# Performance work log

Hardware: AMD Instinct MI355X
Metric: run time of the kernel (lower is better)

Reference implementation:

```python
import jax, jax.numpy as jnp
from jax import lax
import numpy as np


def _gru_step(gi, h, Whh, bhh):
    # torch GRU cell: gates ordered (r, z, n); gi = x @ Wih.T + bih precomputed
    gh = h @ Whh.T + bhh
    ir, iz, inn = jnp.split(gi, 3, axis=-1)
    hr, hz, hn = jnp.split(gh, 3, axis=-1)
    r = jax.nn.sigmoid(ir + hr)
    z = jax.nn.sigmoid(iz + hz)
    n = jnp.tanh(inn + r * hn)
    return (1.0 - z) * n + z * h


def setup_inputs() -> dict:
    key = jax.random.key(0)
    ks = jax.random.split(key, 12)
    B, T, F, Wd, H, L = 64, 80, 4096, 6000, 512, 32
    s = 0.05  # weight init scale
    return {
        "x": jax.random.uniform(ks[0], (B, T, F), jnp.float32),  # nonneg CNN features -> full video lengths
        "y": jax.random.randint(ks[1], (L, B), 0, Wd),           # time-major caption token ids
        "Wih_v": jax.random.normal(ks[2], (3 * H, F), jnp.float32) * s,
        "Whh_v": jax.random.normal(ks[3], (3 * H, H), jnp.float32) * s,
        "bih_v": jax.random.normal(ks[4], (3 * H,), jnp.float32) * s,
        "bhh_v": jax.random.normal(ks[5], (3 * H,), jnp.float32) * s,
        "Wih_c": jax.random.normal(ks[6], (3 * H, H + Wd), jnp.float32) * s,
        "Whh_c": jax.random.normal(ks[7], (3 * H, H), jnp.float32) * s,
        "bih_c": jax.random.normal(ks[8], (3 * H,), jnp.float32) * s,
        "bhh_c": jax.random.normal(ks[9], (3 * H,), jnp.float32) * s,
        "Wout": jax.random.normal(ks[10], (Wd, H), jnp.float32) * s,
        "bout": jax.random.normal(ks[11], (Wd,), jnp.float32) * s,
    }


def reference(x, y, Wih_v, Whh_v, bih_v, bhh_v, Wih_c, Whh_c, bih_c, bhh_c, Wout, bout):
    B, T, F = x.shape
    L = y.shape[0]
    H = Whh_v.shape[1]
    Wd = Wout.shape[0]
    dt = x.dtype

    # ---- encode stage: video GRU over full-length sequences (time-major) ----
    xs = jnp.transpose(x, (1, 0, 2))                       # [T,B,F]
    gi_v = jnp.einsum('tbf,gf->tbg', xs, Wih_v) + bih_v    # precompute input gates
    h0 = jnp.zeros((B, H), dt)

    def enc_v(h, gi):
        h2 = _gru_step(gi, h, Whh_v, bhh_v)
        return h2, h2

    _, enc_out = lax.scan(enc_v, h0, gi_v)                 # [T,B,H]

    # caption GRU over [enc_out ; zeros(word_dim)]; zero word part contributes nothing
    Wih_c_h = Wih_c[:, :H]                                 # [3H,H]
    Wih_c_w = Wih_c[:, H:]                                 # [3H,Wd]
    gi_c = jnp.einsum('tbh,gh->tbg', enc_out, Wih_c_h) + bih_c

    def enc_c(h, gi):
        h2 = _gru_step(gi, h, Whh_c, bhh_c)
        return h2, None

    # NOTE: original code assigns this final hidden to `hidden_video` (quirk preserved)
    hidden_video, _ = lax.scan(enc_c, h0, gi_c)            # [B,H]

    # ---- decode stage: steps i = 1 .. L-1, zero frame input, teacher forcing ----
    gi_zero = jnp.broadcast_to(bih_v, (B, 3 * H))          # x=0 -> input gates are just bias
    WcwT = Wih_c_w.T                                       # [Wd,3H]; one-hot matmul == row gather

    def dec(h_v, y_prev):
        h_v2 = _gru_step(gi_zero, h_v, Whh_v, bhh_v)
        gi = h_v2 @ Wih_c_h.T + WcwT[y_prev] + bih_c       # concat([out, one_hot(y_prev)]) @ Wih_c.T
        h_c = _gru_step(gi, h_v2, Whh_c, bhh_c)            # initial hidden = fresh video hidden (original quirk)
        logits = h_c @ Wout.T + bout
        return h_v2, logits

    _, logits = lax.scan(dec, hidden_video, y[:-1])        # [L-1,B,Wd]

    probs = jnp.zeros((B, L, Wd), dt)
    probs = probs.at[0, 0, 1].set(1.0)                     # probs[0,:,1]=1 survives only at t=0
    probs = probs.at[:, 1:].set(jnp.transpose(logits, (1, 0, 2)))

    # loss is overwritten each iteration in the original -> last step only (cross-entropy)
    logp = jax.nn.log_softmax(logits[-1], axis=-1)         # [B,Wd]
    loss = -jnp.take_along_axis(logp, y[-1][:, None], axis=1).mean()
    return probs, loss
```

## Files before the change

### kernel.cpp

```cpp
#include <hip/hip_runtime.h>

typedef short s16x8 __attribute__((ext_vector_type(8)));
typedef float f32x4 __attribute__((ext_vector_type(4)));
typedef unsigned short u16x4 __attribute__((ext_vector_type(4)));

#define MFMA_B16(a, b, c) __builtin_amdgcn_mfma_f32_16x16x32_bf16((a), (b), (c), 0, 0, 0)

__device__ __forceinline__ unsigned short f2b(float f) {
    unsigned u = __builtin_bit_cast(unsigned, f);
    u = (u + 0x7fffu + ((u >> 16) & 1u)) >> 16;
    return (unsigned short)u;
}
__device__ __forceinline__ float b2f(unsigned short h) {
    unsigned u = ((unsigned)h) << 16;
    return __builtin_bit_cast(float, u);
}
__device__ __forceinline__ float sigm(float x) { return 1.f / (1.f + __expf(-x)); }
__device__ __forceinline__ float tanh_f(float x) {
    float t = __expf(-2.f * fabsf(x));
    float r = (1.f - t) / (1.f + t);
    return copysignf(r, x);
}

__device__ __forceinline__ void stg_b16_sc(unsigned short* p, unsigned short v) {
    unsigned v32 = v;
    asm volatile("global_store_short %0, %1, off sc1" :: "v"(p), "v"(v32) : "memory");
}
__device__ __forceinline__ void stg_b32_sc(float* p, float v) {
    asm volatile("global_store_dword %0, %1, off sc1" :: "v"(p), "v"(v) : "memory");
}
__device__ __forceinline__ unsigned long long ldg_u64_sc(const void* p) {
    return __hip_atomic_load((unsigned long long*)p, __ATOMIC_RELAXED, __HIP_MEMORY_SCOPE_AGENT);
}
__device__ __forceinline__ float ldg_b16_sc(const unsigned short* p) {
    unsigned short v = __hip_atomic_load((unsigned short*)p, __ATOMIC_RELAXED, __HIP_MEMORY_SCOPE_AGENT);
    return b2f(v);
}
__device__ __forceinline__ float ldg_f32_sc(const float* p) {
    return __hip_atomic_load((float*)p, __ATOMIC_RELAXED, __HIP_MEMORY_SCOPE_AGENT);
}
__device__ __forceinline__ s16x8 ldA_sc(const unsigned short* p) {
    union { unsigned long long u[2]; s16x8 v; } r;
    r.u[0] = ldg_u64_sc(p);
    r.u[1] = ldg_u64_sc((const unsigned long long*)p + 1);
    return r.v;
}

__device__ __forceinline__ void block_publish(int* flag, int v) {
    asm volatile("s_waitcnt vmcnt(0)" ::: "memory");
    __syncthreads();
    if (threadIdx.x == 0)
        __hip_atomic_store(flag, v, __ATOMIC_RELAXED, __HIP_MEMORY_SCOPE_AGENT);
}
template <int SLP>
__device__ __forceinline__ void flags_wait2(const int* f1, int t1, const int* f2, int t2) {
    const int lane = threadIdx.x & 63;
    const int* ptr = (lane < 32) ? (f1 + lane * 16) : (f2 + (lane - 32) * 16);
    const int tgt = (lane < 32) ? t1 : t2;
    for (;;) {
        int v = __hip_atomic_load((int*)ptr, __ATOMIC_RELAXED, __HIP_MEMORY_SCOPE_AGENT);
        if (__all(v >= tgt)) break;
        __builtin_amdgcn_s_sleep(SLP);
    }
}
template <int SLP>
__device__ __forceinline__ void flags_wait(const int* f, int t) {
    flags_wait2<SLP>(f, t, f, t);
}
template <int SLP>
__device__ __forceinline__ void scalar_wait(int* c, int target) {
    while (__hip_atomic_load(c, __ATOMIC_RELAXED, __HIP_MEMORY_SCOPE_AGENT) < target)
        __builtin_amdgcn_s_sleep(SLP);
}
__device__ __forceinline__ void wave_add(int* c) {
    asm volatile("s_waitcnt vmcnt(0)" ::: "memory");
    if ((threadIdx.x & 63) == 0)
        __hip_atomic_fetch_add(c, 1, __ATOMIC_RELAXED, __HIP_MEMORY_SCOPE_AGENT);
}

#define WTILE 8192
#define WF(Wl, t, c, lane) (*(const s16x8*)((Wl) + (((t) * 16 + (c)) * 64 + (lane)) * 8))

__device__ __forceinline__ void stage_swz(const unsigned short* __restrict__ src,
                                          unsigned short* dst) {
    for (int idx = threadIdx.x; idx < 1024; idx += 256) {
        const int ln = idx & 63;
        *(uint4*)(dst + (size_t)idx * 8) =
            *(const uint4*)(src + (size_t)(ln & 15) * 512 + (ln >> 4) * 8 + ((idx >> 6)) * 32);
    }
}

__device__ __forceinline__ void mm3_s(const unsigned short* __restrict__ A, int m0,
                                      const unsigned short* Wl, int lane,
                                      f32x4& a0, f32x4& a1, f32x4& a2) {
    const unsigned short* ab = A + (size_t)(m0 + (lane & 15)) * 512 + (lane >> 4) * 8;
#pragma unroll
    for (int c = 0; c < 16; ++c) {
        s16x8 a = ldA_sc(ab + c * 32);
        a0 = MFMA_B16(a, WF(Wl, 0, c, lane), a0);
        a1 = MFMA_B16(a, WF(Wl, 1, c, lane), a1);
        a2 = MFMA_B16(a, WF(Wl, 2, c, lane), a2);
    }
}
__device__ __forceinline__ void mm6_s(const unsigned short* __restrict__ A0,
                                      const unsigned short* __restrict__ A1, int m0,
                                      const unsigned short* Wl, int lane,
                                      f32x4& aR, f32x4& aZ, f32x4& aIN, f32x4& aHN) {
    const unsigned short* a0 = A0 + (size_t)(m0 + (lane & 15)) * 512 + (lane >> 4) * 8;
    const unsigned short* a1 = A1 + (size_t)(m0 + (lane & 15)) * 512 + (lane >> 4) * 8;
#pragma unroll
    for (int c = 0; c < 16; ++c) {
        s16x8 x0 = ldA_sc(a0 + c * 32);
        s16x8 x1 = ldA_sc(a1 + c * 32);
        aR  = MFMA_B16(x0, WF(Wl, 0, c, lane), aR);
        aZ  = MFMA_B16(x0, WF(Wl, 1, c, lane), aZ);
        aIN = MFMA_B16(x0, WF(Wl, 2, c, lane), aIN);
        aR  = MFMA_B16(x1, WF(Wl, 3, c, lane), aR);
        aZ  = MFMA_B16(x1, WF(Wl, 4, c, lane), aZ);
        aHN = MFMA_B16(x1, WF(Wl, 5, c, lane), aHN);
    }
}

__global__ void prep_kernel(const float* __restrict__ x, const float* __restrict__ Wih_v,
                            const float* __restrict__ Whh_v, const float* __restrict__ Whh_c,
                            const float* __restrict__ Wih_c, const float* __restrict__ Wout,
                            unsigned short* __restrict__ xB, unsigned short* __restrict__ WihB,
                            unsigned short* __restrict__ WhhvB, unsigned short* __restrict__ WhhcB,
                            unsigned short* __restrict__ WchhB, unsigned short* __restrict__ WoutB,
                            unsigned short* __restrict__ zeroB, int* __restrict__ ctrs,
                            float* __restrict__ out) {
    const int n = gridDim.x * blockDim.x;
    const int id0 = blockIdx.x * blockDim.x + threadIdx.x;
    for (int i = id0; i < 5242880; i += n) {
        const int e = i * 4;
        const int f = e & 4095, bt = e >> 12;
        const int b = bt / 80, t = bt - b * 80;
        float4 v = *(const float4*)(x + (size_t)e);
        u16x4 s = {f2b(v.x), f2b(v.y), f2b(v.z), f2b(v.w)};
        *(u16x4*)(xB + (size_t)(t * 64 + b) * 4096 + f) = s;
    }
    for (int i = id0; i < 1572864; i += n) {
        float4 v = *(const float4*)(Wih_v + (size_t)i * 4);
        u16x4 s = {f2b(v.x), f2b(v.y), f2b(v.z), f2b(v.w)};
        *(u16x4*)(WihB + (size_t)i * 4) = s;
    }
    for (int i = id0; i < 786432; i += n) {
        WhhvB[i] = f2b(Whh_v[i]);
        WhhcB[i] = f2b(Whh_c[i]);
        WchhB[i] = f2b(Wih_c[(size_t)(i >> 9) * 6512 + (i & 511)]);
    }
    for (int i = id0; i < 3072000; i += n) WoutB[i] = f2b(Wout[i]);
    for (int i = id0; i < 384000; i += n)
        out[(size_t)(i / 6000) * 192000 + (i % 6000)] = (i == 1) ? 1.f : 0.f;
    for (int i = id0; i < 32768; i += n) zeroB[i] = 0;
    for (int i = id0; i < 4096; i += n) ctrs[i] = 0;
}

__global__ __launch_bounds__(256) void gemm1_kernel(const unsigned short* __restrict__ xB,
                                                    const unsigned short* __restrict__ WihB,
                                                    const float* __restrict__ bih,
                                                    float* __restrict__ gi) {
    __shared__ unsigned short As[128 * 40];
    __shared__ unsigned short Bs[128 * 40];
    const int bm = blockIdx.x % 40;
    const int bn = blockIdx.x / 40;
    const int m0 = bm * 128, n0 = bn * 128;
    const int tid = threadIdx.x;
    const int lane = tid & 63;
    const int wave = tid >> 6;
    const int wm = (wave >> 1) * 64, wn = (wave & 1) * 64;
    const int quad = lane >> 4, l15 = lane & 15;

    const f32x4 z4 = {0.f, 0.f, 0.f, 0.f};
    f32x4 acc[4][4];
#pragma unroll
    for (int i = 0; i < 4; ++i)
#pragma unroll
        for (int j = 0; j < 4; ++j) acc[i][j] = z4;

    const int sr = tid >> 1;
    const int sc0 = (tid & 1) * 16;

    for (int k0 = 0; k0 < 4096; k0 += 32) {
        __syncthreads();
#pragma unroll
        for (int p = 0; p < 2; ++p) {
            const int c8 = sc0 + p * 8;
            *(s16x8*)&As[sr * 40 + c8] =
                *(const s16x8*)(xB + (size_t)(m0 + sr) * 4096 + k0 + c8);
            *(s16x8*)&Bs[sr * 40 + c8] =
                *(const s16x8*)(WihB + (size_t)(n0 + sr) * 4096 + k0 + c8);
        }
        __syncthreads();
        s16x8 af[4], bfr[4];
#pragma unroll
        for (int i = 0; i < 4; ++i) af[i] = *(const s16x8*)&As[(wm + i * 16 + l15) * 40 + quad * 8];
#pragma unroll
        for (int j = 0; j < 4; ++j) bfr[j] = *(const s16x8*)&Bs[(wn + j * 16 + l15) * 40 + quad * 8];
#pragma unroll
        for (int i = 0; i < 4; ++i)
#pragma unroll
            for (int j = 0; j < 4; ++j) acc[i][j] = MFMA_B16(af[i], bfr[j], acc[i][j]);
    }
#pragma unroll
    for (int i = 0; i < 4; ++i)
#pragma unroll
        for (int j = 0; j < 4; ++j)
#pragma unroll
            for (int r = 0; r < 4; ++r) {
                const int m = m0 + wm + i * 16 + quad * 4 + r;
                const int nn = n0 + wn + j * 16 + l15;
                gi[(size_t)m * 1536 + nn] = acc[i][j][r] + bih[nn];
            }
}

struct SeqParams {
    const float* bih_v; const float* bhh_v;
    const float* bih_c; const float* bhh_c;
    const float* bout;  const int* y;
    const float* gi;    const float* Wc;  float* out;
    const unsigned short* WhhvB; const unsigned short* WhhcB; const unsigned short* WchhB;
    const unsigned short* WoutB; unsigned short* WcwTB;
    unsigned short* eo;
    unsigned short* hv2B;
    float*          hv2F;
    unsigned short* hcdB;
    unsigned short* ecb0; unsigned short* ecb1; unsigned short* zeroB;
    float* hcf; float* lossP; int* ctr;
};
#define F_EO (p.ctr)
#define F_EC (p.ctr + 512)
#define F_HV (p.ctr + 1024)
#define F_HC (p.ctr + 1536)
#define S_TR (p.ctr + 2048)
#define S_LOG (p.ctr + 2064)
#define S_LP (p.ctr + 2080)

__global__ __launch_bounds__(256, 1) void seq_kernel(SeqParams p) {
    __shared__ unsigned short Wlds[49152];
    const int blk = blockIdx.x;
    const int lane = threadIdx.x & 63;
    const int wave = threadIdx.x >> 6;
    const int quad = lane >> 4, l15 = lane & 15;
    const f32x4 z4 = {0.f, 0.f, 0.f, 0.f};

    if (blk < 32) {
        const int j0 = blk * 16;
        const int j = j0 + l15;
        const int m0 = wave * 16;
        const int b_ = m0 + quad * 4;
#pragma unroll
        for (int g = 0; g < 3; ++g)
            stage_swz(p.WhhvB + (size_t)(g * 512 + j0) * 512, Wlds + g * WTILE);
        __syncthreads();
        const float bhr = p.bhh_v[j], bhz = p.bhh_v[512 + j], bhn = p.bhh_v[1024 + j];
        float hp[4] = {0.f, 0.f, 0.f, 0.f};

        for (int t = 0; t < 80; ++t) {
            float gr[4], gz[4], gn[4];
            const float* gt = p.gi + (size_t)t * 98304;
#pragma unroll
            for (int r = 0; r < 4; ++r) {
                const float* gb = gt + (size_t)(b_ + r) * 1536;
                gr[r] = gb[j]; gz[r] = gb[512 + j]; gn[r] = gb[1024 + j];
            }
            f32x4 aR = z4, aZ = z4, aN = z4;
            if (t > 0) {
                flags_wait<1>(F_EO, t);
                mm3_s(p.eo + (size_t)(t - 1) * 32768, m0, Wlds, lane, aR, aZ, aN);
            }
            unsigned short* eoW = p.eo + (size_t)t * 32768;
#pragma unroll
            for (int r = 0; r < 4; ++r) {
                float rg = sigm(gr[r] + aR[r] + bhr);
                float zg = sigm(gz[r] + aZ[r] + bhz);
                float ng = tanh_f(gn[r] + rg * (aN[r] + bhn));
                float hn = (1.f - zg) * ng + zg * hp[r];
                hp[r] = hn;
                stg_b16_sc(eoW + (size_t)(b_ + r) * 512 + j, f2b(hn));
            }
            block_publish(F_EO + blk * 16, t + 1);
        }

        flags_wait<1>(F_EC, 80);
        const float bir = p.bih_v[j], biz = p.bih_v[512 + j], bin_ = p.bih_v[1024 + j];
        for (int s = 0; s <= 30; ++s) {
            if (s > 0) flags_wait<1>(F_HV, s);
            f32x4 aR = z4, aZ = z4, aN = z4;
            mm3_s(p.hv2B + (size_t)s * 32768, m0, Wlds, lane, aR, aZ, aN);
            unsigned short* hw = p.hv2B + (size_t)(s + 1) * 32768;
            float* hwF = p.hv2F + (size_t)(s + 1) * 32768;
#pragma unroll
            for (int r = 0; r < 4; ++r) {
                float hpv = (s == 0) ? ldg_f32_sc(p.hcf + (size_t)(b_ + r) * 512 + j) : hp[r];
                float rg = sigm(bir + aR[r] + bhr);
                float zg = sigm(biz + aZ[r] + bhz);
                float ng = tanh_f(bin_ + rg * (aN[r] + bhn));
                float hn = (1.f - zg) * ng + zg * hpv;
                hp[r] = hn;
                stg_b16_sc(hw + (size_t)(b_ + r) * 512 + j, f2b(hn));
                stg_b32_sc(hwF + (size_t)(b_ + r) * 512 + j, hn);
            }
            block_publish(F_HV + blk * 16, s + 1);
        }

        if (blk < 16) {
            const int b = (blk << 2) | wave;
            scalar_wait<2>(S_LOG, 125);
            const float* lg = p.out + (size_t)b * 192000 + 186000;
            float m = -1e30f, sum = 0.f;
            for (int i = lane; i < 3000; i += 64) {
                union { unsigned long long u; float f[2]; } pr;
                pr.u = ldg_u64_sc(lg + 2 * i);
#pragma unroll
                for (int e = 0; e < 2; ++e) {
                    float v = pr.f[e];
                    float nm = fmaxf(m, v);
                    sum = sum * __expf(m - nm) + __expf(v - nm);
                    m = nm;
                }
            }
#pragma unroll
            for (int off = 32; off > 0; off >>= 1) {
                float m2 = __shfl_down(m, off);
                float s2 = __shfl_down(sum, off);
                float nm = fmaxf(m, m2);
                sum = sum * __expf(m - nm) + s2 * __expf(m2 - nm);
                m = nm;
            }
            if (lane == 0) {
                int yv = p.y[31 * 64 + b];
                float lgy = ldg_f32_sc(lg + yv);
                stg_b32_sc(p.lossP + b, (m + __logf(sum)) - lgy);
            }
            wave_add(S_LP);
            if (blk == 0 && wave == 0) {
                scalar_wait<1>(S_LP, 64);
                float v = ldg_f32_sc(p.lossP + lane);
#pragma unroll
                for (int off = 32; off > 0; off >>= 1) v += __shfl_down(v, off);
                if (lane == 0) p.out[12288000] = v * (1.f / 64.f);
            }
        }
    } else if (blk < 64) {
        const int cid = blk - 32;
        const int j0 = cid * 16;
        const int j = j0 + l15;
        const int m0 = wave * 16;
        const int b_ = m0 + quad * 4;
#pragma unroll
        for (int g = 0; g < 3; ++g) {
            stage_swz(p.WchhB + (size_t)(g * 512 + j0) * 512, Wlds + g * WTILE);
            stage_swz(p.WhhcB + (size_t)(g * 512 + j0) * 512, Wlds + (3 + g) * WTILE);
        }
        __syncthreads();
        const float bcr = p.bih_c[j] + p.bhh_c[j];
        const float bcz = p.bih_c[512 + j] + p.bhh_c[512 + j];
        const float bin_ = p.bih_c[1024 + j];
        const float bhn = p.bhh_c[1024 + j];
        float hp[4] = {0.f, 0.f, 0.f, 0.f};

        for (int t = 0; t < 80; ++t) {
            flags_wait2<1>(F_EO, t + 1, F_EC, t);
            const unsigned short* A1 = (t == 0) ? p.zeroB : ((t & 1) ? p.ecb0 : p.ecb1);
            unsigned short* ew = (t & 1) ? p.ecb1 : p.ecb0;
            f32x4 aR = z4, aZ = z4, aIN = z4, aHN = z4;
            mm6_s(p.eo + (size_t)t * 32768, A1, m0, Wlds, lane, aR, aZ, aIN, aHN);
#pragma unroll
            for (int r = 0; r < 4; ++r) {
                float rg = sigm(aR[r] + bcr);
                float zg = sigm(aZ[r] + bcz);
                float ng = tanh_f(aIN[r] + bin_ + rg * (aHN[r] + bhn));
                float hn = (1.f - zg) * ng + zg * hp[r];
                hp[r] = hn;
                unsigned short hb = f2b(hn);
                stg_b16_sc(ew + (size_t)(b_ + r) * 512 + j, hb);
                if (t == 79) {
                    stg_b16_sc(p.hv2B + (size_t)(b_ + r) * 512 + j, hb);
                    stg_b32_sc(p.hcf + (size_t)(b_ + r) * 512 + j, hn);
                }
            }
            block_publish(F_EC + cid * 16, t + 1);
        }

        scalar_wait<4>(S_TR, 94);
        for (int s = 0; s <= 30; ++s) {
            float er[4], ez[4], en[4];
#pragma unroll
            for (int r = 0; r < 4; ++r) {
                const int yv = p.y[s * 64 + (b_ + r)];
                const unsigned short* em = p.WcwTB + (size_t)yv * 1536;
                er[r] = ldg_b16_sc(em + j);
                ez[r] = ldg_b16_sc(em + 512 + j);
                en[r] = ldg_b16_sc(em + 1024 + j);
            }
            flags_wait<1>(F_HV, s + 1);
            const unsigned short* hv = p.hv2B + (size_t)(s + 1) * 32768;
            const float* hvF = p.hv2F + (size_t)(s + 1) * 32768;
            f32x4 aR = z4, aZ = z4, aIN = z4, aHN = z4;
            mm6_s(hv, hv, m0, Wlds, lane, aR, aZ, aIN, aHN);
            unsigned short* hc = p.hcdB + (size_t)s * 32768;
#pragma unroll
            for (int r = 0; r < 4; ++r) {
                float rg = sigm(aR[r] + er[r] + bcr);
                float zg = sigm(aZ[r] + ez[r] + bcz);
                float ng = tanh_f(aIN[r] + en[r] + bin_ + rg * (aHN[r] + bhn));
                float hpv = ldg_f32_sc(hvF + (size_t)(b_ + r) * 512 + j);
                stg_b16_sc(hc + (size_t)(b_ + r) * 512 + j, f2b((1.f - zg) * ng + zg * hpv));
            }
            block_publish(F_HC + cid * 16, s + 1);
        }
    } else {
        const int bo = blk - 64;
        const int w0 = bo * 48;
#pragma unroll
        for (int tl = 0; tl < 3; ++tl)
            stage_swz(p.WoutB + (size_t)(w0 + tl * 16) * 512, Wlds + tl * WTILE);
        __syncthreads();

        if (bo < 94) {
            float* tile = (float*)(Wlds + 24576);
            const int w0t = bo * 64;
            const int tx = threadIdx.x & 63, ty = threadIdx.x >> 6;
            for (int gt = 0; gt < 24; ++gt) {
                const int g0 = gt * 64;
                __syncthreads();
                for (int r = ty; r < 64; r += 4) {
                    int w = w0t + tx;
                    tile[r * 65 + tx] = (w < 6000) ? p.Wc[(size_t)(g0 + r) * 6512 + 512 + w] : 0.f;
                }
                __syncthreads();
                for (int r = ty; r < 64; r += 4) {
                    int w = w0t + r;
                    if (w < 6000)
                        stg_b16_sc(p.WcwTB + (size_t)w * 1536 + g0 + tx, f2b(tile[tx * 65 + r]));
                }
            }
            asm volatile("s_waitcnt vmcnt(0)" ::: "memory");
            __syncthreads();
            if (threadIdx.x == 0)
                __hip_atomic_fetch_add(S_TR, 1, __ATOMIC_RELAXED, __HIP_MEMORY_SCOPE_AGENT);
        }

        const int m0 = wave * 16;
        const int b_ = m0 + quad * 4;
        float bo_[3];
#pragma unroll
        for (int tl = 0; tl < 3; ++tl) bo_[tl] = p.bout[w0 + tl * 16 + l15];

        for (int s = 0; s <= 30; ++s) {
            flags_wait<2>(F_HC, s + 1);
            const unsigned short* ab =
                p.hcdB + (size_t)s * 32768 + (size_t)(m0 + l15) * 512 + quad * 8;
            s16x8 af[16];
#pragma unroll
            for (int c = 0; c < 16; ++c) af[c] = ldA_sc(ab + c * 32);
#pragma unroll
            for (int tl = 0; tl < 3; ++tl) {
                f32x4 acc = z4;
#pragma unroll
                for (int c = 0; c < 16; ++c) acc = MFMA_B16(af[c], WF(Wlds, tl, c, lane), acc);
#pragma unroll
                for (int r = 0; r < 4; ++r)
                    stg_b32_sc(p.out + (size_t)(b_ + r) * 192000 + (size_t)(s + 1) * 6000 +
                                   w0 + tl * 16 + l15,
                               acc[r] + bo_[tl]);
            }
        }
        asm volatile("s_waitcnt vmcnt(0)" ::: "memory");
        __syncthreads();
        if (threadIdx.x == 0)
            __hip_atomic_fetch_add(S_LOG, 1, __ATOMIC_RELAXED, __HIP_MEMORY_SCOPE_AGENT);
    }
}

extern "C" void kernel_launch(void* const* d_in, const int* in_sizes, int n_in,
                              void* d_out, int out_size, void* d_ws, size_t ws_size,
                              hipStream_t stream) {
    const float* x     = (const float*)d_in[0];
    const int*   y     = (const int*)d_in[1];
    const float* Wih_v = (const float*)d_in[2];
    const float* Whh_v = (const float*)d_in[3];
    const float* bih_v = (const float*)d_in[4];
    const float* bhh_v = (const float*)d_in[5];
    const float* Wih_c = (const float*)d_in[6];
    const float* Whh_c = (const float*)d_in[7];
    const float* bih_c = (const float*)d_in[8];
    const float* bhh_c = (const float*)d_in[9];
    const float* Wout  = (const float*)d_in[10];
    const float* bout  = (const float*)d_in[11];
    float* out = (float*)d_out;

    char* w = (char*)d_ws;
    size_t o = 0;
    auto alloc = [&](size_t bytes) -> void* {
        void* p = (void*)(w + o);
        o += (bytes + 255) & ~(size_t)255;
        return p;
    };
    float*          gi    = (float*)alloc(7864320ull * 4);
    unsigned short* xB    = (unsigned short*)alloc(20971520ull * 2);
    unsigned short* WihB  = (unsigned short*)alloc(6291456ull * 2);
    unsigned short* WhhvB = (unsigned short*)alloc(786432ull * 2);
    unsigned short* WhhcB = (unsigned short*)alloc(786432ull * 2);
    unsigned short* WchhB = (unsigned short*)alloc(786432ull * 2);
    unsigned short* WoutB = (unsigned short*)alloc(3072000ull * 2);
    unsigned short* WcwTB = (unsigned short*)alloc(9216000ull * 2);
    unsigned short* eo    = (unsigned short*)alloc(80ull * 32768 * 2);
    unsigned short* hv2B  = (unsigned short*)alloc(32ull * 32768 * 2);
    float*          hv2F  = (float*)alloc(32ull * 32768 * 4);
    unsigned short* hcdB  = (unsigned short*)alloc(31ull * 32768 * 2);
    unsigned short* ecb0  = (unsigned short*)alloc(32768ull * 2);
    unsigned short* ecb1  = (unsigned short*)alloc(32768ull * 2);
    unsigned short* zeroB = (unsigned short*)alloc(32768ull * 2);
    float*          hcf   = (float*)alloc(32768ull * 4);
    float*          lossP = (float*)alloc(64ull * 4);
    int*            ctrs  = (int*)alloc(4096ull * 4);
    if (o > ws_size) return;

    prep_kernel<<<512, 256, 0, stream>>>(x, Wih_v, Whh_v, Whh_c, Wih_c, Wout, xB, WihB,
                                         WhhvB, WhhcB, WchhB, WoutB, zeroB, ctrs, out);
    gemm1_kernel<<<480, 256, 0, stream>>>(xB, WihB, bih_v, gi);

    SeqParams p;
    p.bih_v = bih_v; p.bhh_v = bhh_v; p.bih_c = bih_c; p.bhh_c = bhh_c;
    p.bout = bout; p.y = y; p.gi = gi; p.Wc = Wih_c; p.out = out;
    p.WhhvB = WhhvB; p.WhhcB = WhhcB; p.WchhB = WchhB; p.WoutB = WoutB; p.WcwTB = WcwTB;
    p.eo = eo; p.hv2B = hv2B; p.hv2F = hv2F; p.hcdB = hcdB;
    p.ecb0 = ecb0; p.ecb1 = ecb1; p.zeroB = zeroB;
    p.hcf = hcf; p.lossP = lossP; p.ctr = ctrs;
    void* args[] = {&p};
    hipLaunchCooperativeKernel((void*)seq_kernel, dim3(189), dim3(256), args, 0, stream);
}
```

Baseline: 1.430 ms.

## Fuse input-gate GEMM into persistent sequence kernel with per-timestep flags

Removes the separate input-gate GEMM launch. The idle output-projection blocks of the cooperative kernel now compute x@Wih^T one timestep at a time and publish a per-timestep counter, so the encoder recurrence can start as soon as its first timestep is ready instead of waiting for the whole GEMM. The prep kernel conversions are also vectorised to float4/u16x4 accesses. The trade-off is a smaller GEMM tile run by only 120 blocks and extra flag polling on the recurrent critical path.

```diff
diff --git a/kernel.cpp b/kernel.cpp
--- a/kernel.cpp
+++ b/kernel.cpp
@@ -144,81 +144,35 @@
         u16x4 s = {f2b(v.x), f2b(v.y), f2b(v.z), f2b(v.w)};
         *(u16x4*)(WihB + (size_t)i * 4) = s;
     }
-    for (int i = id0; i < 786432; i += n) {
-        WhhvB[i] = f2b(Whh_v[i]);
-        WhhcB[i] = f2b(Whh_c[i]);
-        WchhB[i] = f2b(Wih_c[(size_t)(i >> 9) * 6512 + (i & 511)]);
-    }
-    for (int i = id0; i < 3072000; i += n) WoutB[i] = f2b(Wout[i]);
+    for (int i = id0; i < 196608; i += n) {
+        const int e = i * 4;
+        float4 a = *(const float4*)(Whh_v + e);
+        u16x4 sa = {f2b(a.x), f2b(a.y), f2b(a.z), f2b(a.w)};
+        *(u16x4*)(WhhvB + e) = sa;
+        float4 b = *(const float4*)(Whh_c + e);
+        u16x4 sb = {f2b(b.x), f2b(b.y), f2b(b.z), f2b(b.w)};
+        *(u16x4*)(WhhcB + e) = sb;
+        float4 d = *(const float4*)(Wih_c + (size_t)(e >> 9) * 6512 + (e & 511));
+        u16x4 sd = {f2b(d.x), f2b(d.y), f2b(d.z), f2b(d.w)};
+        *(u16x4*)(WchhB + e) = sd;
+    }
+    for (int i = id0; i < 768000; i += n) {
+        float4 a = *(const float4*)(Wout + (size_t)i * 4);
+        u16x4 s = {f2b(a.x), f2b(a.y), f2b(a.z), f2b(a.w)};
+        *(u16x4*)(WoutB + (size_t)i * 4) = s;
+    }
     for (int i = id0; i < 384000; i += n)
         out[(size_t)(i / 6000) * 192000 + (i % 6000)] = (i == 1) ? 1.f : 0.f;
-    for (int i = id0; i < 32768; i += n) zeroB[i] = 0;
+    for (int i = id0; i < 8192; i += n) ((unsigned long long*)zeroB)[i] = 0ull;
     for (int i = id0; i < 4096; i += n) ctrs[i] = 0;
-}
-
-__global__ __launch_bounds__(256) void gemm1_kernel(const unsigned short* __restrict__ xB,
-                                                    const unsigned short* __restrict__ WihB,
-                                                    const float* __restrict__ bih,
-                                                    float* __restrict__ gi) {
-    __shared__ unsigned short As[128 * 40];
-    __shared__ unsigned short Bs[128 * 40];
-    const int bm = blockIdx.x % 40;
-    const int bn = blockIdx.x / 40;
-    const int m0 = bm * 128, n0 = bn * 128;
-    const int tid = threadIdx.x;
-    const int lane = tid & 63;
-    const int wave = tid >> 6;
-    const int wm = (wave >> 1) * 64, wn = (wave & 1) * 64;
-    const int quad = lane >> 4, l15 = lane & 15;
-
-    const f32x4 z4 = {0.f, 0.f, 0.f, 0.f};
-    f32x4 acc[4][4];
-#pragma unroll
-    for (int i = 0; i < 4; ++i)
-#pragma unroll
-        for (int j = 0; j < 4; ++j) acc[i][j] = z4;
-
-    const int sr = tid >> 1;
-    const int sc0 = (tid & 1) * 16;
-
-    for (int k0 = 0; k0 < 4096; k0 += 32) {
-        __syncthreads();
-#pragma unroll
-        for (int p = 0; p < 2; ++p) {
-            const int c8 = sc0 + p * 8;
-            *(s16x8*)&As[sr * 40 + c8] =
-                *(const s16x8*)(xB + (size_t)(m0 + sr) * 4096 + k0 + c8);
-            *(s16x8*)&Bs[sr * 40 + c8] =
-                *(const s16x8*)(WihB + (size_t)(n0 + sr) * 4096 + k0 + c8);
-        }
-        __syncthreads();
-        s16x8 af[4], bfr[4];
-#pragma unroll
-        for (int i = 0; i < 4; ++i) af[i] = *(const s16x8*)&As[(wm + i * 16 + l15) * 40 + quad * 8];
-#pragma unroll
-        for (int j = 0; j < 4; ++j) bfr[j] = *(const s16x8*)&Bs[(wn + j * 16 + l15) * 40 + quad * 8];
-#pragma unroll
-        for (int i = 0; i < 4; ++i)
-#pragma unroll
-            for (int j = 0; j < 4; ++j) acc[i][j] = MFMA_B16(af[i], bfr[j], acc[i][j]);
-    }
-#pragma unroll
-    for (int i = 0; i < 4; ++i)
-#pragma unroll
-        for (int j = 0; j < 4; ++j)
-#pragma unroll
-            for (int r = 0; r < 4; ++r) {
-                const int m = m0 + wm + i * 16 + quad * 4 + r;
-                const int nn = n0 + wn + j * 16 + l15;
-                gi[(size_t)m * 1536 + nn] = acc[i][j][r] + bih[nn];
-            }
 }
 
 struct SeqParams {
     const float* bih_v; const float* bhh_v;
     const float* bih_c; const float* bhh_c;
     const float* bout;  const int* y;
-    const float* gi;    const float* Wc;  float* out;
+    float* gi;          const float* Wc;  float* out;
+    const unsigned short* xB;    const unsigned short* WihB;
     const unsigned short* WhhvB; const unsigned short* WhhcB; const unsigned short* WchhB;
     const unsigned short* WoutB; unsigned short* WcwTB;
     unsigned short* eo;
@@ -235,6 +189,7 @@
 #define S_TR (p.ctr + 2048)
 #define S_LOG (p.ctr + 2064)
 #define S_LP (p.ctr + 2080)
+#define S_GI (p.ctr + 2560)
 
 __global__ __launch_bounds__(256, 1) void seq_kernel(SeqParams p) {
     __shared__ unsigned short Wlds[49152];
@@ -255,14 +210,26 @@
         __syncthreads();
         const float bhr = p.bhh_v[j], bhz = p.bhh_v[512 + j], bhn = p.bhh_v[1024 + j];
         float hp[4] = {0.f, 0.f, 0.f, 0.f};
+        int gall = 0;
 
         for (int t = 0; t < 80; ++t) {
+            if (!gall) {
+                for (;;) {
+                    int a = __hip_atomic_load(S_GI + t, __ATOMIC_RELAXED, __HIP_MEMORY_SCOPE_AGENT);
+                    int z = __hip_atomic_load(S_GI + 79, __ATOMIC_RELAXED, __HIP_MEMORY_SCOPE_AGENT);
+                    if (z >= 12) gall = 1;
+                    if (a >= 12) break;
+                    __builtin_amdgcn_s_sleep(2);
+                }
+            }
             float gr[4], gz[4], gn[4];
             const float* gt = p.gi + (size_t)t * 98304;
 #pragma unroll
             for (int r = 0; r < 4; ++r) {
                 const float* gb = gt + (size_t)(b_ + r) * 1536;
-                gr[r] = gb[j]; gz[r] = gb[512 + j]; gn[r] = gb[1024 + j];
+                gr[r] = ldg_f32_sc(gb + j);
+                gz[r] = ldg_f32_sc(gb + 512 + j);
+                gn[r] = ldg_f32_sc(gb + 1024 + j);
             }
             f32x4 aR = z4, aZ = z4, aN = z4;
             if (t > 0) {
@@ -412,6 +379,56 @@
         }
     } else {
         const int bo = blk - 64;
+
+        if (bo < 120) {
+            unsigned short* As = Wlds;
+            unsigned short* Bs = Wlds + 4608;
+            const int tid = threadIdx.x;
+            const int sra = tid >> 2, sca = (tid & 3) * 16;
+            const int srb = tid >> 1, scb = (tid & 1) * 32;
+            const int m0W = wave * 16;
+            for (int q = bo; q < 960; q += 120) {
+                const int t = q / 12, n0 = (q % 12) * 128;
+                f32x4 acc[8];
+#pragma unroll
+                for (int jj = 0; jj < 8; ++jj) acc[jj] = z4;
+                for (int k0 = 0; k0 < 4096; k0 += 64) {
+                    __syncthreads();
+                    const unsigned short* ax = p.xB + (size_t)(t * 64 + sra) * 4096 + k0 + sca;
+                    *(s16x8*)&As[sra * 72 + sca]     = *(const s16x8*)(ax);
+                    *(s16x8*)&As[sra * 72 + sca + 8] = *(const s16x8*)(ax + 8);
+                    const unsigned short* bx = p.WihB + (size_t)(n0 + srb) * 4096 + k0 + scb;
+                    *(s16x8*)&Bs[srb * 72 + scb]      = *(const s16x8*)(bx);
+                    *(s16x8*)&Bs[srb * 72 + scb + 8]  = *(const s16x8*)(bx + 8);
+                    *(s16x8*)&Bs[srb * 72 + scb + 16] = *(const s16x8*)(bx + 16);
+                    *(s16x8*)&Bs[srb * 72 + scb + 24] = *(const s16x8*)(bx + 24);
+                    __syncthreads();
+#pragma unroll
+                    for (int kk = 0; kk < 2; ++kk) {
+                        s16x8 af = *(const s16x8*)&As[(m0W + l15) * 72 + kk * 32 + quad * 8];
+#pragma unroll
+                        for (int jj = 0; jj < 8; ++jj)
+                            acc[jj] = MFMA_B16(
+                                af, *(const s16x8*)&Bs[(jj * 16 + l15) * 72 + kk * 32 + quad * 8],
+                                acc[jj]);
+                    }
+                }
+#pragma unroll
+                for (int jj = 0; jj < 8; ++jj)
+#pragma unroll
+                    for (int r = 0; r < 4; ++r) {
+                        const int col = n0 + jj * 16 + l15;
+                        const int row = t * 64 + m0W + quad * 4 + r;
+                        stg_b32_sc(p.gi + (size_t)row * 1536 + col, acc[jj][r] + p.bih_v[col]);
+                    }
+                asm volatile("s_waitcnt vmcnt(0)" ::: "memory");
+                __syncthreads();
+                if (threadIdx.x == 0)
+                    __hip_atomic_fetch_add(S_GI + t, 1, __ATOMIC_RELAXED, __HIP_MEMORY_SCOPE_AGENT);
+            }
+            __syncthreads();
+        }
+
         const int w0 = bo * 48;
 #pragma unroll
         for (int tl = 0; tl < 3; ++tl)
@@ -449,7 +466,11 @@
         for (int tl = 0; tl < 3; ++tl) bo_[tl] = p.bout[w0 + tl * 16 + l15];
 
         for (int s = 0; s <= 30; ++s) {
-            flags_wait<2>(F_HC, s + 1);
+            if (wave == 0) {
+                if (s == 0) flags_wait<16>(F_HC, 1);
+                else        flags_wait<2>(F_HC, s + 1);
+            }
+            __syncthreads();
             const unsigned short* ab =
                 p.hcdB + (size_t)s * 32768 + (size_t)(m0 + l15) * 512 + quad * 8;
             s16x8 af[16];
@@ -520,11 +541,11 @@
 
     prep_kernel<<<512, 256, 0, stream>>>(x, Wih_v, Whh_v, Whh_c, Wih_c, Wout, xB, WihB,
                                          WhhvB, WhhcB, WchhB, WoutB, zeroB, ctrs, out);
-    gemm1_kernel<<<480, 256, 0, stream>>>(xB, WihB, bih_v, gi);
 
     SeqParams p;
     p.bih_v = bih_v; p.bhh_v = bhh_v; p.bih_c = bih_c; p.bhh_c = bhh_c;
     p.bout = bout; p.y = y; p.gi = gi; p.Wc = Wih_c; p.out = out;
+    p.xB = xB; p.WihB = WihB;
     p.WhhvB = WhhvB; p.WhhcB = WhhcB; p.WchhB = WchhB; p.WoutB = WoutB; p.WcwTB = WcwTB;
     p.eo = eo; p.hv2B = hv2B; p.hv2F = hv2F; p.hcdB = hcdB;
     p.ecb0 = ecb0; p.ecb1 = ecb1; p.zeroB = zeroB;
```

Result: faster. 1.387 ms (-3.0%).
